# Kernel optimization log

Measured on AMD Instinct MI355X. Metric: run time of the kernel, lower is better.

Reference implementation:

```python
import jax, jax.numpy as jnp
import numpy as np

SIZE = 32            # resize target from size=(32,32)
CAL_THRESH = 0.3
WIN = 11             # standard SSIM gaussian window
SIGMA = 1.5
C1 = (0.01 * 255.0) ** 2   # data range 255 (patches are raw pixel values)
C2 = (0.03 * 255.0) ** 2


def _gauss_window():
    g = np.exp(-((np.arange(WIN) - WIN // 2) ** 2) / (2.0 * SIGMA ** 2))
    g = g / g.sum()
    return jnp.asarray(np.outer(g, g), jnp.float32)


def _gconv(x, win):
    # depthwise gaussian blur, same padding; x: [N,C,H,W]
    C = x.shape[1]
    k = jnp.tile(win[None, None], (C, 1, 1, 1))
    return jax.lax.conv_general_dilated(
        x, k, (1, 1), 'SAME',
        dimension_numbers=('NCHW', 'OIHW', 'NCHW'), feature_group_count=C)


def _crop_resize(img, box):
    # img: [C,H,W]; box: [x,y,w,h] with (x,y) = top-left (as used by the crop).
    # Equivalent to img[:, int(y):int(y+h), int(x):int(x+w)] then bilinear
    # F.interpolate to (SIZE,SIZE), align_corners=False (edge-clamped).
    C, H, W = img.shape
    x0 = jnp.floor(box[0]); y0 = jnp.floor(box[1])
    w = jnp.floor(box[0] + box[2]) - x0   # int(x+w) - int(x)
    h = jnp.floor(box[1] + box[3]) - y0
    ys = jnp.clip((jnp.arange(SIZE, dtype=jnp.float32) + 0.5) * (h / SIZE) - 0.5,
                  0.0, jnp.maximum(h - 1.0, 0.0))
    xs = jnp.clip((jnp.arange(SIZE, dtype=jnp.float32) + 0.5) * (w / SIZE) - 0.5,
                  0.0, jnp.maximum(w - 1.0, 0.0))
    yf = jnp.floor(ys); xf = jnp.floor(xs)
    wy = (ys - yf)[None, :, None]   # row weights
    wx = (xs - xf)[None, None, :]   # col weights

    def gi(yi, xi):
        yi = jnp.clip(yi, 0, H - 1).astype(jnp.int32)
        xi = jnp.clip(xi, 0, W - 1).astype(jnp.int32)
        return img[:, yi[:, None], xi[None, :]]  # [C,SIZE,SIZE]

    ylo = yf + y0; yhi = jnp.minimum(yf + 1.0, jnp.maximum(h - 1.0, 0.0)) + y0
    xlo = xf + x0; xhi = jnp.minimum(xf + 1.0, jnp.maximum(w - 1.0, 0.0)) + x0
    top = gi(ylo, xlo) * (1.0 - wx) + gi(ylo, xhi) * wx
    bot = gi(yhi, xlo) * (1.0 - wx) + gi(yhi, xhi) * wx
    return top * (1.0 - wy) + bot * wy


def _pairwise_iou(gt, pr):
    # faithful to get_two_box_iou: (x,y) treated as CENTER here (source quirk)
    g = gt[:, :, None, :]; p = pr[:, None, :, :]
    tl = jnp.maximum(g[..., :2] - g[..., 2:] / 2, p[..., :2] - p[..., 2:] / 2)
    br = jnp.minimum(g[..., :2] + g[..., 2:] / 2, p[..., :2] + p[..., 2:] / 2)
    en = jnp.prod((tl < br).astype(gt.dtype), axis=-1)
    area_i = jnp.prod(br - tl, axis=-1) * en
    area_g = jnp.prod(gt[..., 2:], axis=-1)[:, :, None]
    area_p = jnp.prod(pr[..., 2:], axis=-1)[:, None, :]
    return area_i / (area_g + area_p - area_i + 1e-16)  # [B,G,P]


def setup_inputs() -> dict:
    key = jax.random.key(0)
    k1, k2, k3, k4, k5 = jax.random.split(key, 5)
    B, G, P, H, W = 8, 16, 64, 640, 640
    imgs = jax.random.uniform(k1, (B, 3, H, W), jnp.float32) * 255.0
    xy = jax.random.uniform(k2, (B, G, 2), jnp.float32) * (W - 80.0) + 4.0
    wh = jax.random.uniform(k3, (B, G, 2), jnp.float32) * 56.0 + 8.0
    gt_boxes = jnp.concatenate([xy, wh], axis=-1)
    base = jnp.tile(gt_boxes, (1, P // G, 1))  # preds jittered around GTs so IoU>thresh often
    jit_xy = jax.random.uniform(k4, (B, P, 2), jnp.float32, -4.0, 4.0)
    jit_wh = jax.random.uniform(k5, (B, P, 2), jnp.float32, -4.0, 4.0)
    pred_boxes = jnp.concatenate(
        [base[..., :2] + jit_xy, jnp.maximum(base[..., 2:] + jit_wh, 3.0)], axis=-1)
    return {"gt_boxes": gt_boxes, "pred_boxes": pred_boxes, "imgs": imgs}


def reference(gt_boxes, pred_boxes, imgs):
    B, G = gt_boxes.shape[:2]; P = pred_boxes.shape[1]
    crop = jax.vmap(jax.vmap(_crop_resize, in_axes=(None, 0)), in_axes=(0, 0))
    gt_patch = crop(imgs, gt_boxes)     # [B,G,3,S,S]
    pr_patch = crop(imgs, pred_boxes)   # [B,P,3,S,S]

    iou = _pairwise_iou(gt_boxes, pred_boxes)                    # [B,G,P]
    valid = (pred_boxes[..., 2] > 2) & (pred_boxes[..., 3] > 2)  # [B,P]
    mask = ((iou > CAL_THRESH) & valid[:, None, :]).astype(imgs.dtype)

    # surviving pairs -> dense pair grid (masked mean == mean over survivors)
    x = jnp.broadcast_to(pr_patch[:, None], (B, G, P, 3, SIZE, SIZE)).reshape(-1, 3, SIZE, SIZE)
    y = jnp.broadcast_to(gt_patch[:, :, None], (B, G, P, 3, SIZE, SIZE)).reshape(-1, 3, SIZE, SIZE)

    win = _gauss_window()
    mu1 = _gconv(x, win); mu2 = _gconv(y, win)
    mu1_sq = mu1 * mu1; mu2_sq = mu2 * mu2; mu12 = mu1 * mu2
    s1 = _gconv(x * x, win) - mu1_sq
    s2 = _gconv(y * y, win) - mu2_sq
    s12 = _gconv(x * y, win) - mu12
    ssim_map = ((2 * mu12 + C1) * (2 * s12 + C2)) / ((mu1_sq + mu2_sq + C1) * (s1 + s2 + C2))

    loss = jnp.abs(x / 255.0 - y / 255.0) + (1.0 - ssim_map)    # L1 + SSIM loss, [N,3,S,S]
    loss = loss.reshape(B, G, P, 3, SIZE, SIZE)
    m = mask[:, :, :, None, None, None]
    cnt = jnp.sum(mask) * (3 * SIZE * SIZE)
    total = jnp.sum(loss * m)
    return jnp.where(cnt > 0, total / jnp.maximum(cnt, 1.0), 0.0)
```

## Files before the change

kernel.cpp:

```cpp
#include <hip/hip_runtime.h>
#include <math.h>

#define TSIZE 32
#define WIN 11
#define NB 8
#define NG 16
#define NP 64
#define IMH 640
#define IMW 640
#define NBOX 640
#define NPAIR 8192
#define NCOMP (NPAIR/256)
#define K2GRID 1536

#define C1F 6.5025f
#define C2F 58.5225f

#define SWZ4(row, jq) (((row) << 5) + ((((jq) + (row)) & 7) << 2))

struct GaussW { float g[WIN]; };
struct f4 { float v[4]; };

__device__ __forceinline__ float shl(float v, int src) {
    src = src < 0 ? 0 : (src > 63 ? 63 : src);
    return __shfl(v, src, 64);
}

__device__ __forceinline__ void row_window(
    const float* __restrict__ own, int lane, int t, float* __restrict__ pv)
{
    const int l = lane;
    const float a0 = shl(own[0], l - 1), a1 = shl(own[1], l - 1);
    const float a2 = shl(own[2], l - 1), a3 = shl(own[3], l - 1);
    const float b0 = shl(own[0], l + 1), b1 = shl(own[1], l + 1);
    const float b2 = shl(own[2], l + 1), b3 = shl(own[3], l + 1);
    const float m3 = shl(own[3], l - 2);
    const float p0 = shl(own[0], l + 2);
    const bool vm1 = (t >= 1), vm2 = (t >= 2);
    const bool vp1 = (t <= 6), vp2 = (t <= 5);
    pv[0]  = vm2 ? m3 : 0.0f;
    pv[1]  = vm1 ? a0 : 0.0f;
    pv[2]  = vm1 ? a1 : 0.0f;
    pv[3]  = vm1 ? a2 : 0.0f;
    pv[4]  = vm1 ? a3 : 0.0f;
    pv[5]  = own[0]; pv[6] = own[1]; pv[7] = own[2]; pv[8] = own[3];
    pv[9]  = vp1 ? b0 : 0.0f;
    pv[10] = vp1 ? b1 : 0.0f;
    pv[11] = vp1 ? b2 : 0.0f;
    pv[12] = vp1 ? b3 : 0.0f;
    pv[13] = vp2 ? p0 : 0.0f;
}

__global__ __launch_bounds__(256) void gen_patches(
    const float* __restrict__ gt_boxes, const float* __restrict__ pred_boxes,
    const float* __restrict__ imgs,
    float* __restrict__ patches, float* __restrict__ mus, float* __restrict__ gsqs,
    int* __restrict__ pair_list, int* __restrict__ pair_cnt, GaussW gw)
{
    const int bid = blockIdx.x;
    const int tid = threadIdx.x;

    if (bid >= NBOX * 3) {
        const int blk = bid - NBOX * 3;
        const int p = blk * 256 + tid;
        const int b  = p >> 10;
        const int gi = (p >> 6) & 15;
        const int pi = p & 63;
        bool mask;
        {
#pragma clang fp contract(off)
            const float* gb = gt_boxes  + ((size_t)b * NG + gi) * 4;
            const float* pb = pred_boxes + ((size_t)b * NP + pi) * 4;
            const float gx = gb[0], gy = gb[1], gw_ = gb[2], gh = gb[3];
            const float px = pb[0], py = pb[1], pw = pb[2], ph = pb[3];
            const float tlx = fmaxf(gx - gw_ / 2.0f, px - pw / 2.0f);
            const float tly = fmaxf(gy - gh / 2.0f, py - ph / 2.0f);
            const float brx = fminf(gx + gw_ / 2.0f, px + pw / 2.0f);
            const float bry = fminf(gy + gh / 2.0f, py + ph / 2.0f);
            const float en = ((tlx < brx) ? 1.0f : 0.0f) * ((tly < bry) ? 1.0f : 0.0f);
            const float ai = ((brx - tlx) * (bry - tly)) * en;
            const float ag = gw_ * gh;
            const float ap = pw * ph;
            const float iou = ai / (ag + ap - ai + 1e-16f);
            mask = (iou > 0.3f) && (pw > 2.0f) && (ph > 2.0f);
        }
        __shared__ int wcnt[4], woff[4];
        const unsigned long long bal = __ballot(mask);
        const int lane = tid & 63, wid = tid >> 6;
        if (lane == 0) wcnt[wid] = __popcll(bal);
        __syncthreads();
        if (tid == 0) {
            int s = 0;
#pragma unroll
            for (int w = 0; w < 4; ++w) { woff[w] = s; s += wcnt[w]; }
            pair_cnt[blk] = s;
        }
        __syncthreads();
        if (mask) {
            const int pre = __popcll(bal & ((1ull << lane) - 1ull));
            pair_list[blk * 256 + woff[wid] + pre] = p;
        }
        return;
    }

    const int box = bid / 3;
    const int c   = bid - box * 3;
    int b;
    const float* boxp;
    if (box < NB * NG) {
        b = box >> 4;
        boxp = gt_boxes + (size_t)box * 4;
    } else {
        const int q = box - NB * NG;
        b = q >> 6;
        boxp = pred_boxes + (size_t)q * 4;
    }
    const float* __restrict__ ic = imgs + ((size_t)b * 3 + c) * (IMH * IMW);
    float* __restrict__ patch_o = patches + ((size_t)box * 3 + c) * 1024;
    float* __restrict__ mu_o    = mus     + ((size_t)box * 3 + c) * 1024;
    float* __restrict__ gsq_o   = gsqs    + ((size_t)box * 3 + c) * 1024;

    __shared__ int   s_ylo[TSIZE], s_yhi[TSIZE], s_xlo[TSIZE], s_xhi[TSIZE];
    __shared__ float s_wy[TSIZE], s_wx[TSIZE];
    __shared__ __align__(16) float smem[4704];
    float* const ta = smem;
    float* const tb = smem + 1024;

    {
#pragma clang fp contract(off)
        const float b0 = boxp[0], b1 = boxp[1], b2 = boxp[2], b3 = boxp[3];
        const float x0 = floorf(b0), y0 = floorf(b1);
        const float w = floorf(b0 + b2) - x0;
        const float h = floorf(b1 + b3) - y0;

        if (tid < TSIZE) {
            const int t = tid;
            const float hm = fmaxf(h - 1.0f, 0.0f);
            const float scale = h / 32.0f;
            float ys = ((float)t + 0.5f) * scale - 0.5f;
            ys = fminf(fmaxf(ys, 0.0f), hm);
            const float yf = floorf(ys);
            s_wy[t] = ys - yf;
            const float ylo = yf + y0;
            const float yhi = fminf(yf + 1.0f, hm) + y0;
            s_ylo[t] = (int)fminf(fmaxf(ylo, 0.0f), (float)(IMH - 1));
            s_yhi[t] = (int)fminf(fmaxf(yhi, 0.0f), (float)(IMH - 1));
        } else if (tid < 2 * TSIZE) {
            const int t = tid - TSIZE;
            const float wm = fmaxf(w - 1.0f, 0.0f);
            const float scale = w / 32.0f;
            float xs = ((float)t + 0.5f) * scale - 0.5f;
            xs = fminf(fmaxf(xs, 0.0f), wm);
            const float xf = floorf(xs);
            s_wx[t] = xs - xf;
            const float xlo = xf + x0;
            const float xhi = fminf(xf + 1.0f, wm) + x0;
            s_xlo[t] = (int)fminf(fmaxf(xlo, 0.0f), (float)(IMW - 1));
            s_xhi[t] = (int)fminf(fmaxf(xhi, 0.0f), (float)(IMW - 1));
        }
    }
    __syncthreads();

    const int ry0 = s_ylo[0], ry1 = s_yhi[31];
    const int rx0 = s_xlo[0], rx1 = s_xhi[31];
    const int RH = ry1 - ry0 + 1;
    const int RW = rx1 - rx0 + 1;
    const int stride = RW | 1;
    const int wv = tid >> 6, lane = tid & 63;
    {
        float rbuf[17];
        const bool cl = lane < RW;
#pragma unroll
        for (int u = 0; u < 17; ++u) {
            const int r = wv + (u << 2);
            rbuf[u] = (r < RH && cl)
                      ? ic[(size_t)(ry0 + r) * IMW + rx0 + lane] : 0.0f;
        }
        const bool c2 = (64 + lane) < RW;
#pragma unroll
        for (int u = 0; u < 17; ++u) {
            const int r = wv + (u << 2);
            if (r < RH) {
                if (cl) smem[r * stride + lane] = rbuf[u];
                if (c2) smem[r * stride + 64 + lane] =
                            ic[(size_t)(ry0 + r) * IMW + rx0 + 64 + lane];
            }
        }
    }
    __syncthreads();

    const int i  = tid >> 3;
    const int t  = tid & 7;
    const int j4 = t << 2;
    const int jq = t;
    const int e4 = (i << 5) + j4;

    float vv[4];
    {
        const int yl = s_ylo[i] - ry0, yh = s_yhi[i] - ry0;
        const float wy = s_wy[i];
#pragma unroll
        for (int q = 0; q < 4; ++q) {
#pragma clang fp contract(off)
            const int j = j4 + q;
            const int xl = s_xlo[j] - rx0, xh = s_xhi[j] - rx0;
            const float wx = s_wx[j];
            const float tl = smem[yl * stride + xl], tr = smem[yl * stride + xh];
            const float bl = smem[yh * stride + xl], br = smem[yh * stride + xh];
            const float top = tl * (1.0f - wx) + tr * wx;
            const float bot = bl * (1.0f - wx) + br * wx;
            vv[q] = top * (1.0f - wy) + bot * wy;
        }
    }
    __syncthreads();

    {
        f4 o; o.v[0] = vv[0]; o.v[1] = vv[1]; o.v[2] = vv[2]; o.v[3] = vv[3];
        *(f4*)&patch_o[e4] = o;
    }

    {
        float pv[14];
        row_window(vv, lane, t, pv);
        float am[4] = {0.f,0.f,0.f,0.f}, aq[4] = {0.f,0.f,0.f,0.f};
#pragma unroll
        for (int k = 0; k < WIN; ++k) {
            const float gk = gw.g[k];
#pragma unroll
            for (int q = 0; q < 4; ++q) {
                const float v = pv[k + q];
                am[q] += gk * v;
                aq[q] += gk * (v * v);
            }
        }
        f4 oa, ob;
#pragma unroll
        for (int q = 0; q < 4; ++q) { oa.v[q] = am[q]; ob.v[q] = aq[q]; }
        *(f4*)&ta[SWZ4(i, jq)] = oa;
        *(f4*)&tb[SWZ4(i, jq)] = ob;
    }
    __syncthreads();

    {
        float cm[4] = {0.f,0.f,0.f,0.f}, cq[4] = {0.f,0.f,0.f,0.f};
#pragma unroll
        for (int k = 0; k < WIN; ++k) {
            const int ii = i - 5 + k;
            if (ii >= 0 && ii < TSIZE) {
                const float gk = gw.g[k];
                const f4 m4 = *(const f4*)&ta[SWZ4(ii, jq)];
                const f4 s4 = *(const f4*)&tb[SWZ4(ii, jq)];
#pragma unroll
                for (int q = 0; q < 4; ++q) {
                    cm[q] += gk * m4.v[q];
                    cq[q] += gk * s4.v[q];
                }
            }
        }
        f4 om, oq;
#pragma unroll
        for (int q = 0; q < 4; ++q) { om.v[q] = cm[q]; oq.v[q] = cq[q]; }
        *(f4*)&mu_o[e4]  = om;
        *(f4*)&gsq_o[e4] = oq;
    }
}

__global__ __launch_bounds__(256) void pair_kernel(
    const float* __restrict__ patches, const float* __restrict__ mus,
    const float* __restrict__ gsqs,
    const int* __restrict__ pair_list, const int* __restrict__ pair_cnt,
    float* __restrict__ partial, GaussW gw)
{
    __shared__ __align__(16) float tp[1024];
    __shared__ float wred[4];
    __shared__ int cum[NCOMP + 1];
    const int tid = threadIdx.x;

    if (tid == 0) {
        int s = 0;
#pragma unroll
        for (int k = 0; k < NCOMP; ++k) { cum[k] = s; s += pair_cnt[k]; }
        cum[NCOMP] = s;
    }
    __syncthreads();
    const int nw = cum[NCOMP] * 3;

    const int i  = tid >> 3;
    const int t  = tid & 7;
    const int j4 = t << 2;
    const int jq = t;
    const int e4 = (i << 5) + j4;
    const int lane = tid & 63;

    for (int w = blockIdx.x; w < nw; w += gridDim.x) {
        const int k3 = w / 3;
        const int c  = w - k3 * 3;
        int s = 0;
        while (cum[s + 1] <= k3) ++s;
        const int p  = pair_list[s * 256 + (k3 - cum[s])];
        const int b  = p >> 10;
        const int gi = (p >> 6) & 15;
        const int pi = p & 63;
        const int gbox = b * NG + gi;
        const int pbox = NB * NG + b * NP + pi;
        const size_t po = ((size_t)pbox * 3 + c) * 1024;
        const size_t go = ((size_t)gbox * 3 + c) * 1024;

        const f4 xv = *(const f4*)&patches[po + e4];
        const f4 yv = *(const f4*)&patches[go + e4];

        {
            float prod[4];
#pragma unroll
            for (int q = 0; q < 4; ++q) prod[q] = xv.v[q] * yv.v[q];
            float pv[14];
            row_window(prod, lane, t, pv);
            float a[4] = {0.f,0.f,0.f,0.f};
#pragma unroll
            for (int k = 0; k < WIN; ++k) {
                const float gk = gw.g[k];
#pragma unroll
                for (int q = 0; q < 4; ++q) a[q] += gk * pv[k + q];
            }
            f4 o;
#pragma unroll
            for (int q = 0; q < 4; ++q) o.v[q] = a[q];
            *(f4*)&tp[SWZ4(i, jq)] = o;
        }
        __syncthreads();

        float lsum = 0.0f;
        {
            float cxy[4] = {0.f,0.f,0.f,0.f};
#pragma unroll
            for (int k = 0; k < WIN; ++k) {
                const int ii = i - 5 + k;
                if (ii >= 0 && ii < TSIZE) {
                    const float gk = gw.g[k];
                    const f4 t4 = *(const f4*)&tp[SWZ4(ii, jq)];
#pragma unroll
                    for (int q = 0; q < 4; ++q) cxy[q] += gk * t4.v[q];
                }
            }
            const f4 mu1 = *(const f4*)&mus[po + e4];
            const f4 mu2 = *(const f4*)&mus[go + e4];
            const f4 q1  = *(const f4*)&gsqs[po + e4];
            const f4 q2  = *(const f4*)&gsqs[go + e4];
#pragma unroll
            for (int q = 0; q < 4; ++q) {
                const float m1 = mu1.v[q], m2 = mu2.v[q];
                const float m1s = m1 * m1, m2s = m2 * m2, m12 = m1 * m2;
                const float s1  = q1.v[q] - m1s;
                const float s2  = q2.v[q] - m2s;
                const float s12 = cxy[q] - m12;
                const float num = (2.0f * m12 + C1F) * (2.0f * s12 + C2F);
                const float den = (m1s + m2s + C1F) * (s1 + s2 + C2F);
                const float ssim = num / den;
                lsum += fabsf(xv.v[q] / 255.0f - yv.v[q] / 255.0f) + (1.0f - ssim);
            }
        }

#pragma unroll
        for (int off = 32; off > 0; off >>= 1) lsum += __shfl_down(lsum, off);
        if (lane == 0) wred[tid >> 6] = lsum;
        __syncthreads();
        if (tid == 0) partial[w] = wred[0] + wred[1] + wred[2] + wred[3];
        __syncthreads();
    }
}

__global__ __launch_bounds__(256) void finalize_kernel(
    const int* __restrict__ pair_cnt, const float* __restrict__ partial,
    float* __restrict__ out)
{
    __shared__ float wred[4];
    const int tid = threadIdx.x;
    int n = 0;
#pragma unroll
    for (int k = 0; k < NCOMP; ++k) n += pair_cnt[k];
    const int nw = n * 3;
    float lsum = 0.0f;
    for (int w = tid; w < nw; w += 256) lsum += partial[w];
#pragma unroll
    for (int off = 32; off > 0; off >>= 1) lsum += __shfl_down(lsum, off);
    if ((tid & 63) == 0) wred[tid >> 6] = lsum;
    __syncthreads();
    if (tid == 0) {
        const float total = wred[0] + wred[1] + wred[2] + wred[3];
        out[0] = (n > 0) ? (total / ((float)n * 3072.0f)) : 0.0f;
    }
}

extern "C" void kernel_launch(void* const* d_in, const int* in_sizes, int n_in,
                              void* d_out, int out_size, void* d_ws, size_t ws_size,
                              hipStream_t stream) {
    const float* gt_boxes   = (const float*)d_in[0];
    const float* pred_boxes = (const float*)d_in[1];
    const float* imgs       = (const float*)d_in[2];

    GaussW gw;
    {
        double gd[WIN]; double s = 0.0;
        for (int k = 0; k < WIN; ++k) {
            const double d = (double)(k - WIN / 2);
            gd[k] = exp(-(d * d) / (2.0 * 1.5 * 1.5));
            s += gd[k];
        }
        for (int k = 0; k < WIN; ++k) gw.g[k] = (float)(gd[k] / s);
    }

    float* ws = (float*)d_ws;
    float* patches = ws;
    float* mus     = patches + (size_t)NBOX * 3072;
    float* gsqs    = mus     + (size_t)NBOX * 3072;
    float* partial = gsqs    + (size_t)NBOX * 3072;
    int* pair_list = (int*)(partial + 3 * NPAIR);
    int* pair_cnt  = pair_list + NPAIR;

    gen_patches<<<NBOX * 3 + NCOMP, 256, 0, stream>>>(
        gt_boxes, pred_boxes, imgs, patches, mus, gsqs, pair_list, pair_cnt, gw);

    pair_kernel<<<K2GRID, 256, 0, stream>>>(
        patches, mus, gsqs, pair_list, pair_cnt, partial, gw);

    finalize_kernel<<<1, 256, 0, stream>>>(pair_cnt, partial, (float*)d_out);
}
```

Before: 101.0 us.

## Fold finalize into pair kernel via per-block atomic accumulation

Removes the separate finalize kernel launch by having each pair_kernel block accumulate its loss across all work items in a register, reduce once at the end, scale by the precomputed inverse count, and atomically add into the output. The output is zeroed inside gen_patches. The serial prefix over pair counts is replaced by a wavefront shuffle scan. The row-prefetch buffer also grows from 17 to 18 rows, which appears to cover a tall-crop edge case. In exchange the float atomics make the summation order nondeterministic, and the partial buffer goes away.

```diff
diff --git a/kernel.cpp b/kernel.cpp
--- a/kernel.cpp
+++ b/kernel.cpp
@@ -55,13 +55,15 @@
     const float* __restrict__ gt_boxes, const float* __restrict__ pred_boxes,
     const float* __restrict__ imgs,
     float* __restrict__ patches, float* __restrict__ mus, float* __restrict__ gsqs,
-    int* __restrict__ pair_list, int* __restrict__ pair_cnt, GaussW gw)
+    int* __restrict__ pair_list, int* __restrict__ pair_cnt,
+    float* __restrict__ out, GaussW gw)
 {
     const int bid = blockIdx.x;
     const int tid = threadIdx.x;
 
     if (bid >= NBOX * 3) {
         const int blk = bid - NBOX * 3;
+        if (blk == 0 && tid == 0) out[0] = 0.0f;
         const int p = blk * 256 + tid;
         const int b  = p >> 10;
         const int gi = (p >> 6) & 15;
@@ -168,17 +170,17 @@
     const int stride = RW | 1;
     const int wv = tid >> 6, lane = tid & 63;
     {
-        float rbuf[17];
+        float rbuf[18];
         const bool cl = lane < RW;
 #pragma unroll
-        for (int u = 0; u < 17; ++u) {
+        for (int u = 0; u < 18; ++u) {
             const int r = wv + (u << 2);
             rbuf[u] = (r < RH && cl)
                       ? ic[(size_t)(ry0 + r) * IMW + rx0 + lane] : 0.0f;
         }
         const bool c2 = (64 + lane) < RW;
 #pragma unroll
-        for (int u = 0; u < 17; ++u) {
+        for (int u = 0; u < 18; ++u) {
             const int r = wv + (u << 2);
             if (r < RH) {
                 if (cl) smem[r * stride + lane] = rbuf[u];
@@ -269,28 +271,36 @@
     const float* __restrict__ patches, const float* __restrict__ mus,
     const float* __restrict__ gsqs,
     const int* __restrict__ pair_list, const int* __restrict__ pair_cnt,
-    float* __restrict__ partial, GaussW gw)
+    float* __restrict__ out, GaussW gw)
 {
     __shared__ __align__(16) float tp[1024];
     __shared__ float wred[4];
     __shared__ int cum[NCOMP + 1];
     const int tid = threadIdx.x;
-
-    if (tid == 0) {
-        int s = 0;
-#pragma unroll
-        for (int k = 0; k < NCOMP; ++k) { cum[k] = s; s += pair_cnt[k]; }
-        cum[NCOMP] = s;
-    }
-    __syncthreads();
-    const int nw = cum[NCOMP] * 3;
+    const int lane = tid & 63;
+
+    if (tid < 64) {
+        int v = (lane < NCOMP) ? pair_cnt[lane] : 0;
+#pragma unroll
+        for (int d = 1; d < 32; d <<= 1) {
+            const int u = __shfl_up(v, d, 64);
+            if ((lane & 31) >= d) v += u;
+        }
+        if (lane < NCOMP) cum[lane + 1] = v;
+        if (lane == 0) cum[0] = 0;
+    }
+    __syncthreads();
+    const int n  = cum[NCOMP];
+    const int nw = n * 3;
+    const float inv_den = (n > 0) ? 1.0f / ((float)n * 3072.0f) : 0.0f;
 
     const int i  = tid >> 3;
     const int t  = tid & 7;
     const int j4 = t << 2;
     const int jq = t;
     const int e4 = (i << 5) + j4;
-    const int lane = tid & 63;
+
+    float bsum = 0.0f;
 
     for (int w = blockIdx.x; w < nw; w += gridDim.x) {
         const int k3 = w / 3;
@@ -360,34 +370,17 @@
             }
         }
 
-#pragma unroll
-        for (int off = 32; off > 0; off >>= 1) lsum += __shfl_down(lsum, off);
-        if (lane == 0) wred[tid >> 6] = lsum;
+        bsum += lsum;
         __syncthreads();
-        if (tid == 0) partial[w] = wred[0] + wred[1] + wred[2] + wred[3];
-        __syncthreads();
-    }
-}
-
-__global__ __launch_bounds__(256) void finalize_kernel(
-    const int* __restrict__ pair_cnt, const float* __restrict__ partial,
-    float* __restrict__ out)
-{
-    __shared__ float wred[4];
-    const int tid = threadIdx.x;
-    int n = 0;
-#pragma unroll
-    for (int k = 0; k < NCOMP; ++k) n += pair_cnt[k];
-    const int nw = n * 3;
-    float lsum = 0.0f;
-    for (int w = tid; w < nw; w += 256) lsum += partial[w];
-#pragma unroll
-    for (int off = 32; off > 0; off >>= 1) lsum += __shfl_down(lsum, off);
-    if ((tid & 63) == 0) wred[tid >> 6] = lsum;
+    }
+
+#pragma unroll
+    for (int off = 32; off > 0; off >>= 1) bsum += __shfl_down(bsum, off);
+    if (lane == 0) wred[tid >> 6] = bsum;
     __syncthreads();
     if (tid == 0) {
         const float total = wred[0] + wred[1] + wred[2] + wred[3];
-        out[0] = (n > 0) ? (total / ((float)n * 3072.0f)) : 0.0f;
+        if (total != 0.0f) atomicAdd(out, total * inv_den);
     }
 }
 
@@ -413,15 +406,13 @@
     float* patches = ws;
     float* mus     = patches + (size_t)NBOX * 3072;
     float* gsqs    = mus     + (size_t)NBOX * 3072;
-    float* partial = gsqs    + (size_t)NBOX * 3072;
-    int* pair_list = (int*)(partial + 3 * NPAIR);
+    int* pair_list = (int*)(gsqs + (size_t)NBOX * 3072);
     int* pair_cnt  = pair_list + NPAIR;
 
     gen_patches<<<NBOX * 3 + NCOMP, 256, 0, stream>>>(
-        gt_boxes, pred_boxes, imgs, patches, mus, gsqs, pair_list, pair_cnt, gw);
+        gt_boxes, pred_boxes, imgs, patches, mus, gsqs,
+        pair_list, pair_cnt, (float*)d_out, gw);
 
     pair_kernel<<<K2GRID, 256, 0, stream>>>(
-        patches, mus, gsqs, pair_list, pair_cnt, partial, gw);
-
-    finalize_kernel<<<1, 256, 0, stream>>>(pair_cnt, partial, (float*)d_out);
+        patches, mus, gsqs, pair_list, pair_cnt, (float*)d_out, gw);
 }
```

After: 112.9 us. +11.7%, slower.
